# Kernel tuning notes

Measured on AMD Instinct MI355X. Metric: run time of the kernel, lower is better.

Reference implementation:

```python
import jax, jax.numpy as jnp
import numpy as np

D_MODEL = 2048
NUM_HEADS = 16
D_FF = 8192
BATCH = 4
SEQ = 2048


def setup_inputs() -> dict:
    key = jax.random.key(0)
    ks = jax.random.split(key, 16)
    s_attn = 1.0 / np.sqrt(D_MODEL)
    s_ff1 = 1.0 / np.sqrt(D_MODEL)
    s_ff2 = 1.0 / np.sqrt(D_FF)
    return {
        "x": jax.random.normal(ks[0], (BATCH, SEQ, D_MODEL), dtype=jnp.float32),
        "Wq": jax.random.normal(ks[1], (D_MODEL, D_MODEL), dtype=jnp.float32) * s_attn,
        "bq": jnp.zeros((D_MODEL,), dtype=jnp.float32),
        "Wk": jax.random.normal(ks[2], (D_MODEL, D_MODEL), dtype=jnp.float32) * s_attn,
        "bk": jnp.zeros((D_MODEL,), dtype=jnp.float32),
        "Wv": jax.random.normal(ks[3], (D_MODEL, D_MODEL), dtype=jnp.float32) * s_attn,
        "bv": jnp.zeros((D_MODEL,), dtype=jnp.float32),
        "Wo": jax.random.normal(ks[4], (D_MODEL, D_MODEL), dtype=jnp.float32) * s_attn,
        "bo": jnp.zeros((D_MODEL,), dtype=jnp.float32),
        "W1": jax.random.normal(ks[5], (D_MODEL, D_FF), dtype=jnp.float32) * s_ff1,
        "b1": jnp.zeros((D_FF,), dtype=jnp.float32),
        "W2": jax.random.normal(ks[6], (D_FF, D_MODEL), dtype=jnp.float32) * s_ff2,
        "b2": jnp.zeros((D_MODEL,), dtype=jnp.float32),
        "ln1_g": jnp.ones((D_MODEL,), dtype=jnp.float32),
        "ln1_b": jnp.zeros((D_MODEL,), dtype=jnp.float32),
        "ln2_g": jnp.ones((D_MODEL,), dtype=jnp.float32),
        "ln2_b": jnp.zeros((D_MODEL,), dtype=jnp.float32),
    }


def _layer_norm(x, g, b, eps=1e-5):
    mu = jnp.mean(x, axis=-1, keepdims=True)
    var = jnp.mean(jnp.square(x - mu), axis=-1, keepdims=True)
    return (x - mu) * jax.lax.rsqrt(var + eps) * g + b


def _attention(h, Wq, bq, Wk, bk, Wv, bv, Wo, bo):
    B, S, D = h.shape
    H = NUM_HEADS
    dk = D // H
    q = (h @ Wq + bq).reshape(B, S, H, dk).transpose(0, 2, 1, 3)  # bhsd
    k = (h @ Wk + bk).reshape(B, S, H, dk).transpose(0, 2, 1, 3)
    v = (h @ Wv + bv).reshape(B, S, H, dk).transpose(0, 2, 1, 3)
    logits = jnp.einsum("bhqd,bhkd->bhqk", q, k) / jnp.sqrt(jnp.float32(dk))
    causal = jnp.triu(jnp.ones((S, S), dtype=bool), k=1)  # True above diagonal
    logits = jnp.where(causal, -jnp.inf, logits)
    attn = jax.nn.softmax(logits, axis=-1)
    out = jnp.einsum("bhqk,bhkd->bhqd", attn, v)
    out = out.transpose(0, 2, 1, 3).reshape(B, S, D)
    return out @ Wo + bo


def reference(x, Wq, bq, Wk, bk, Wv, bv, Wo, bo, W1, b1, W2, b2,
              ln1_g, ln1_b, ln2_g, ln2_b):
    # Pre-LN attention block + residual
    h = _layer_norm(x, ln1_g, ln1_b)
    x = x + _attention(h, Wq, bq, Wk, bk, Wv, bv, Wo, bo)
    # Pre-LN FFN block + residual (GELU activation)
    h = _layer_norm(x, ln2_g, ln2_b)
    ff = jax.nn.gelu(h @ W1 + b1, approximate=False) @ W2 + b2
    return x + ff
```

## Files before the change

kernel.cpp:

```cpp
#include <hip/hip_runtime.h>
#include <hip/hip_bf16.h>

#define D_MODEL 2048
#define NUM_HEADS 16
#define D_FF 8192
#define BATCH 4
#define SEQ 2048
#define DK 128
#define MTOT (BATCH * SEQ)

typedef __attribute__((ext_vector_type(8))) short short8;
typedef __attribute__((ext_vector_type(4))) short short4v;
typedef __attribute__((ext_vector_type(4))) float f32x4;

#define MFMA16(a, b, c) __builtin_amdgcn_mfma_f32_16x16x32_bf16(a, b, c, 0, 0, 0)

#define GLOAD16(gp, lp)                                                        \
  __builtin_amdgcn_global_load_lds(                                            \
      (const __attribute__((address_space(1))) void*)(gp),                     \
      (__attribute__((address_space(3))) void*)(lp), 16, 0, 0)

#define SBAR() asm volatile("s_barrier" ::: "memory")

static __device__ __forceinline__ unsigned short f2bf(float f) {
  return __builtin_bit_cast(unsigned short, __float2bfloat16(f));
}

__global__ __launch_bounds__(256) void transpose_cvt_kernel(
    const float* __restrict__ in, __hip_bfloat16* __restrict__ out, int K, int N) {
  __shared__ float tile[32][33];
  const int n0 = blockIdx.x * 32, k0 = blockIdx.y * 32;
  const int tx = threadIdx.x & 31, ty = threadIdx.x >> 5;
#pragma unroll
  for (int i = 0; i < 4; ++i)
    tile[ty + i * 8][tx] = in[(size_t)(k0 + ty + i * 8) * N + n0 + tx];
  __syncthreads();
#pragma unroll
  for (int i = 0; i < 4; ++i)
    out[(size_t)(n0 + ty + i * 8) * K + k0 + tx] = __float2bfloat16(tile[tx][ty + i * 8]);
}

__global__ __launch_bounds__(256) void transpose_cvt4_kernel(
    const float* __restrict__ s0, const float* __restrict__ s1,
    const float* __restrict__ s2, const float* __restrict__ s3,
    __hip_bfloat16* __restrict__ d0, __hip_bfloat16* __restrict__ d1,
    __hip_bfloat16* __restrict__ d2, __hip_bfloat16* __restrict__ d3) {
  const int z = blockIdx.z;
  const float* in = z == 0 ? s0 : (z == 1 ? s1 : (z == 2 ? s2 : s3));
  __hip_bfloat16* out = z == 0 ? d0 : (z == 1 ? d1 : (z == 2 ? d2 : d3));
  __shared__ float tile[32][33];
  const int n0 = blockIdx.x * 32, k0 = blockIdx.y * 32;
  const int tx = threadIdx.x & 31, ty = threadIdx.x >> 5;
#pragma unroll
  for (int i = 0; i < 4; ++i)
    tile[ty + i * 8][tx] = in[(size_t)(k0 + ty + i * 8) * 2048 + n0 + tx];
  __syncthreads();
#pragma unroll
  for (int i = 0; i < 4; ++i)
    out[(size_t)(n0 + ty + i * 8) * 2048 + k0 + tx] =
        __float2bfloat16(tile[tx][ty + i * 8]);
}

__global__ __launch_bounds__(256) void layernorm_kernel(
    const float* __restrict__ x, const float* __restrict__ g,
    const float* __restrict__ bta, __hip_bfloat16* __restrict__ out) {
  const int row = blockIdx.x;
  const int tid = threadIdx.x;
  const float* xr = x + (size_t)row * D_MODEL;
  float4 v0 = *(const float4*)(xr + tid * 8);
  float4 v1 = *(const float4*)(xr + tid * 8 + 4);
  float s = v0.x + v0.y + v0.z + v0.w + v1.x + v1.y + v1.z + v1.w;
  float q = v0.x * v0.x + v0.y * v0.y + v0.z * v0.z + v0.w * v0.w +
            v1.x * v1.x + v1.y * v1.y + v1.z * v1.z + v1.w * v1.w;
#pragma unroll
  for (int off = 1; off < 64; off <<= 1) {
    s += __shfl_xor(s, off);
    q += __shfl_xor(q, off);
  }
  __shared__ float rs[4], rq[4];
  if ((tid & 63) == 0) {
    rs[tid >> 6] = s;
    rq[tid >> 6] = q;
  }
  __syncthreads();
  s = rs[0] + rs[1] + rs[2] + rs[3];
  q = rq[0] + rq[1] + rq[2] + rq[3];
  const float mu = s * (1.0f / D_MODEL);
  const float var = q * (1.0f / D_MODEL) - mu * mu;
  const float rstd = rsqrtf(var + 1e-5f);
  float4 g0 = *(const float4*)(g + tid * 8);
  float4 g1 = *(const float4*)(g + tid * 8 + 4);
  float4 b0 = *(const float4*)(bta + tid * 8);
  float4 b1 = *(const float4*)(bta + tid * 8 + 4);
  short8 o;
  o[0] = (short)f2bf((v0.x - mu) * rstd * g0.x + b0.x);
  o[1] = (short)f2bf((v0.y - mu) * rstd * g0.y + b0.y);
  o[2] = (short)f2bf((v0.z - mu) * rstd * g0.z + b0.z);
  o[3] = (short)f2bf((v0.w - mu) * rstd * g0.w + b0.w);
  o[4] = (short)f2bf((v1.x - mu) * rstd * g1.x + b1.x);
  o[5] = (short)f2bf((v1.y - mu) * rstd * g1.y + b1.y);
  o[6] = (short)f2bf((v1.z - mu) * rstd * g1.z + b1.z);
  o[7] = (short)f2bf((v1.w - mu) * rstd * g1.w + b1.w);
  *(short8*)(out + (size_t)row * D_MODEL + tid * 8) = o;
}

enum { EPI_BF16 = 0, EPI_VT = 1, EPI_RESID = 2, EPI_GELU = 3, EPI_QKV = 4 };

#define AF_MFMA_PHASE(FI0)                                                     \
  {                                                                            \
    const int raA = wm + (FI0) * 16 + l15;                                     \
    const int raB = wm + ((FI0) + 1) * 16 + l15;                               \
    short8 aA0 = *(const short8*)(db + raA * 128 + ((lg ^ (raA & 7)) << 4));   \
    short8 aB0 = *(const short8*)(db + raB * 128 + ((lg ^ (raB & 7)) << 4));   \
    short8 aA1 =                                                               \
        *(const short8*)(db + raA * 128 + (((4 + lg) ^ (raA & 7)) << 4));      \
    short8 aB1 =                                                               \
        *(const short8*)(db + raB * 128 + (((4 + lg) ^ (raB & 7)) << 4));      \
    SBAR();                                                                    \
    asm volatile("s_waitcnt lgkmcnt(0)" ::: "memory");                         \
    __builtin_amdgcn_sched_barrier(0);                                         \
    __builtin_amdgcn_s_setprio(1);                                             \
    _Pragma("unroll") for (int fj = 0; fj < 4; ++fj)                           \
        acc[FI0][fj] = MFMA16(aA0, bf0[fj], acc[FI0][fj]);                     \
    _Pragma("unroll") for (int fj = 0; fj < 4; ++fj)                           \
        acc[(FI0) + 1][fj] = MFMA16(aB0, bf0[fj], acc[(FI0) + 1][fj]);         \
    _Pragma("unroll") for (int fj = 0; fj < 4; ++fj)                           \
        acc[FI0][fj] = MFMA16(aA1, bf1[fj], acc[FI0][fj]);                     \
    _Pragma("unroll") for (int fj = 0; fj < 4; ++fj)                           \
        acc[(FI0) + 1][fj] = MFMA16(aB1, bf1[fj], acc[(FI0) + 1][fj]);         \
    __builtin_amdgcn_s_setprio(0);                                             \
  }

template <int EPI>
__global__ __launch_bounds__(512, 2) void gemm_kernel(
    const __hip_bfloat16* __restrict__ A, const __hip_bfloat16* __restrict__ Bt,
    const float* __restrict__ bias, const float* __restrict__ bias2,
    const float* __restrict__ bias3, const float* __restrict__ resid,
    void* __restrict__ outv, void* __restrict__ out2, void* __restrict__ out3,
    int M, int N, int K) {
  __shared__ __align__(16) unsigned char lds[2][65536];
  const int tid = threadIdx.x;
  const int lane = tid & 63, w = tid >> 6;
  const int l15 = lane & 15, lg = lane >> 4;
  const int d = blockIdx.x;
  const int x = d & 7;
  const int i = d >> 3;
  const int cC = (i & 7) + 8 * (i >> 5);
  const int rC = x + 8 * ((i >> 3) & 3);
  const int m0 = rC * 256, n0 = cC * 256;
  const int wm = (w >> 2) * 128, wn = (w & 3) * 64;

  f32x4 acc[8][4] = {};

  const int row8 = lane >> 3;
  const int g8 = (lane & 7) ^ row8;
  const int wa = (w & 3) + ((w >> 2) * 16);

  auto stA = [&](int tt, int c) {
    GLOAD16(A + (size_t)(m0 + c * 8 + row8) * K + (size_t)tt * 64 + g8 * 8,
            lds[tt & 1] + c * 1024);
  };
  auto stB = [&](int tt, int c) {
    GLOAD16(Bt + (size_t)(n0 + c * 8 + row8) * K + (size_t)tt * 64 + g8 * 8,
            lds[tt & 1] + 32768 + c * 1024);
  };

  const int nt = K >> 6;

  stB(0, w); stB(0, 8 + w); stA(0, wa);
  stB(0, 16 + w); stB(0, 24 + w); stA(0, wa + 4);
  stA(0, wa + 8); stA(0, wa + 12);
  stB(1, w); stB(1, 8 + w); stA(1, wa);
  stB(1, 16 + w); stB(1, 24 + w); stA(1, wa + 4);
  stA(1, wa + 8);
  asm volatile("s_waitcnt vmcnt(7)" ::: "memory");
  SBAR();

  for (int t = 0; t < nt; ++t) {
    const unsigned char* db = lds[t & 1];
    const bool s1 = (t + 1 < nt), s2 = (t + 2 < nt);
    short8 bf0[4], bf1[4];
    if (s1) stA(t + 1, wa + 12);
#pragma unroll
    for (int f = 0; f < 4; ++f) {
      const int rb = wn + f * 16 + l15;
      bf0[f] = *(const short8*)(db + 32768 + rb * 128 + ((lg ^ (rb & 7)) << 4));
      bf1[f] =
          *(const short8*)(db + 32768 + rb * 128 + (((4 + lg) ^ (rb & 7)) << 4));
    }
    AF_MFMA_PHASE(0)
    SBAR();
    if (s2) { stB(t + 2, w); stB(t + 2, 8 + w); stA(t + 2, wa); }
    AF_MFMA_PHASE(2)
    SBAR();
    if (s2) { stB(t + 2, 16 + w); stB(t + 2, 24 + w); stA(t + 2, wa + 4); }
    AF_MFMA_PHASE(4)
    SBAR();
    if (s2) stA(t + 2, wa + 8);
    AF_MFMA_PHASE(6)
    if (s2)
      asm volatile("s_waitcnt vmcnt(7)" ::: "memory");
    else
      asm volatile("s_waitcnt vmcnt(0)" ::: "memory");
    SBAR();
  }

#pragma unroll
  for (int fi = 0; fi < 8; ++fi) {
#pragma unroll
    for (int fj = 0; fj < 4; ++fj) {
      const int mb = m0 + wm + fi * 16 + lg * 4;
      const int n = n0 + wn + fj * 16 + l15;
      if constexpr (EPI == EPI_QKV) {
        const int sec = n >> 11;
        const int nn = n & 2047;
        const float bv = sec == 0 ? bias[nn] : (sec == 1 ? bias2[nn] : bias3[nn]);
        if (sec < 2) {
          __hip_bfloat16* o = sec == 0 ? (__hip_bfloat16*)outv : (__hip_bfloat16*)out2;
#pragma unroll
          for (int r = 0; r < 4; ++r)
            o[(size_t)(mb + r) * 2048 + nn] = __float2bfloat16(acc[fi][fj][r] + bv);
        } else {
          const int bb = mb >> 11, ss = mb & (SEQ - 1);
          const int hh = nn >> 7, dd = nn & (DK - 1);
          short4v pk;
#pragma unroll
          for (int r = 0; r < 4; ++r) pk[r] = (short)f2bf(acc[fi][fj][r] + bv);
          __hip_bfloat16* o = (__hip_bfloat16*)out3;
          *(short4v*)(o + ((size_t)((bb * NUM_HEADS + hh) * DK + dd)) * SEQ + ss) = pk;
        }
      } else {
        const float bv = bias ? bias[n] : 0.0f;
        if constexpr (EPI == EPI_VT) {
          const int bb = mb >> 11, ss = mb & (SEQ - 1);
          const int hh = n >> 7, dd = n & (DK - 1);
          short4v pk;
#pragma unroll
          for (int r = 0; r < 4; ++r) pk[r] = (short)f2bf(acc[fi][fj][r] + bv);
          __hip_bfloat16* o = (__hip_bfloat16*)outv;
          *(short4v*)(o + ((size_t)((bb * NUM_HEADS + hh) * DK + dd)) * SEQ + ss) = pk;
        } else {
#pragma unroll
          for (int r = 0; r < 4; ++r) {
            const int m = mb + r;
            const float v = acc[fi][fj][r] + bv;
            if constexpr (EPI == EPI_BF16) {
              ((__hip_bfloat16*)outv)[(size_t)m * N + n] = __float2bfloat16(v);
            } else if constexpr (EPI == EPI_GELU) {
              const float ge = 0.5f * v * (1.0f + erff(v * 0.70710678118654752f));
              ((__hip_bfloat16*)outv)[(size_t)m * N + n] = __float2bfloat16(ge);
            } else {
              ((float*)outv)[(size_t)m * N + n] = resid[(size_t)m * N + n] + v;
            }
          }
        }
      }
    }
  }
}

__global__ __launch_bounds__(512, 4) void attn_kernel(
    const __hip_bfloat16* __restrict__ Qm, const __hip_bfloat16* __restrict__ Km,
    const __hip_bfloat16* __restrict__ Vt, __hip_bfloat16* __restrict__ Om) {
  __shared__ __align__(16) unsigned char Kl[2][16384];
  __shared__ __align__(16) unsigned char Vl[2][16384];
  const int tid = threadIdx.x;
  const int lane = tid & 63, w = tid >> 6;
  const int l15 = lane & 15, lg = lane >> 4;
  const int bh = blockIdx.y, b = bh >> 4, h = bh & 15;
  const int q0 = ((int)gridDim.x - 1 - (int)blockIdx.x) * 128;
  const int qw = q0 + w * 16;
  const int row8 = lane >> 3;
  const int nt = (q0 >> 6) + 2;

  short8 qf[4];
  const __hip_bfloat16* qbase = Qm + (size_t)(b * SEQ + qw + l15) * D_MODEL + h * DK;
#pragma unroll
  for (int ks = 0; ks < 4; ++ks) qf[ks] = *(const short8*)(qbase + ks * 32 + lg * 8);

  float m_run = -1e30f, l_run = 0.0f;
  f32x4 acc_o[8];
#pragma unroll
  for (int fd = 0; fd < 8; ++fd) acc_o[fd] = (f32x4){0.f, 0.f, 0.f, 0.f};

  auto STAGE = [&](int tt) {
    unsigned char* kb = Kl[tt & 1];
    unsigned char* vb = Vl[tt & 1];
    const int t0s = tt * 64;
#pragma unroll
    for (int i = 0; i < 2; ++i) {
      const int c = w * 2 + i;
      const int row = c * 4 + lg;
      const int gcb = l15 ^ (row & 7);
      GLOAD16(Km + (size_t)(b * SEQ + t0s + row) * D_MODEL + h * DK + gcb * 8,
              kb + c * 1024);
    }
#pragma unroll
    for (int i = 0; i < 2; ++i) {
      const int c = w * 2 + i;
      const int row = c * 8 + row8;
      const int gcb = (lane & 7) ^ (row & 7);
      GLOAD16(Vt + (size_t)(bh * DK + row) * SEQ + t0s + gcb * 8, vb + c * 1024);
    }
  };

  STAGE(0);
  for (int t = 0; t < nt; ++t) {
    const int t0 = t * 64;
    if (t + 1 < nt) {
      STAGE(t + 1);
      asm volatile("s_waitcnt vmcnt(4)" ::: "memory");
    } else {
      asm volatile("s_waitcnt vmcnt(0)" ::: "memory");
    }
    SBAR();
    if (t0 <= qw + 15) {
      const unsigned char* kb = Kl[t & 1];
      const unsigned char* vb = Vl[t & 1];
      f32x4 sacc[4];
#pragma unroll
      for (int fn = 0; fn < 4; ++fn) sacc[fn] = (f32x4){0.f, 0.f, 0.f, 0.f};
      __builtin_amdgcn_s_setprio(1);
#pragma unroll
      for (int ks = 0; ks < 4; ++ks) {
        const int cb = ks * 4 + lg;
#pragma unroll
        for (int fn = 0; fn < 4; ++fn) {
          const int rn = fn * 16 + l15;
          short8 kf = *(const short8*)(kb + rn * 256 + ((cb ^ (rn & 7)) << 4));
          sacc[fn] = MFMA16(kf, qf[ks], sacc[fn]);
        }
      }
      __builtin_amdgcn_s_setprio(0);
      const float scale = 0.088388347648318447f;
      const int qg = qw + l15;
      float mt = -1e30f;
#pragma unroll
      for (int fn = 0; fn < 4; ++fn) {
        const int keyb = t0 + fn * 16 + lg * 4;
#pragma unroll
        for (int r = 0; r < 4; ++r) {
          float sv = sacc[fn][r] * scale;
          sv = (keyb + r <= qg) ? sv : -1e30f;
          sacc[fn][r] = sv;
          mt = fmaxf(mt, sv);
        }
      }
      mt = fmaxf(mt, __shfl_xor(mt, 16));
      mt = fmaxf(mt, __shfl_xor(mt, 32));
      const bool defer = __all(mt <= m_run + 8.0f);
      float alpha = 1.0f;
      if (!defer) {
        const float mnew = fmaxf(m_run, mt);
        alpha = __expf(m_run - mnew);
        m_run = mnew;
      }
      float ls = 0.0f;
#pragma unroll
      for (int fn = 0; fn < 4; ++fn)
#pragma unroll
        for (int r = 0; r < 4; ++r) {
          const float p = __expf(sacc[fn][r] - m_run);
          sacc[fn][r] = p;
          ls += p;
        }
      ls += __shfl_xor(ls, 16);
      ls += __shfl_xor(ls, 32);
      l_run = (defer ? l_run : l_run * alpha) + ls;
      if (!defer) {
        float abr[4];
#pragma unroll
        for (int r = 0; r < 4; ++r) abr[r] = __shfl(alpha, lg * 4 + r);
#pragma unroll
        for (int fd = 0; fd < 8; ++fd)
#pragma unroll
          for (int r = 0; r < 4; ++r) acc_o[fd][r] *= abr[r];
      }
      const int srcLo = l15 + 16 * (2 * (lg & 1));
      const int srcHi = srcLo + 16;
      const int hi = lg >> 1;
#pragma unroll
      for (int s = 0; s < 2; ++s) {
        short8 pf;
#pragma unroll
        for (int j = 0; j < 4; ++j) {
          const float v0 = __shfl(sacc[2 * s][j], srcLo);
          const float v1 = __shfl(sacc[2 * s + 1][j], srcLo);
          pf[j] = (short)f2bf(hi ? v1 : v0);
          const float w0 = __shfl(sacc[2 * s][j], srcHi);
          const float w1 = __shfl(sacc[2 * s + 1][j], srcHi);
          pf[4 + j] = (short)f2bf(hi ? w1 : w0);
        }
        const int cb = s * 4 + lg;
        __builtin_amdgcn_s_setprio(1);
#pragma unroll
        for (int fd = 0; fd < 8; ++fd) {
          const int rv = fd * 16 + l15;
          short8 vf = *(const short8*)(vb + rv * 128 + ((cb ^ (rv & 7)) << 4));
          acc_o[fd] = MFMA16(pf, vf, acc_o[fd]);
        }
        __builtin_amdgcn_s_setprio(0);
      }
    }
    asm volatile("s_waitcnt lgkmcnt(0)" ::: "memory");
    SBAR();
  }
  float linv[4];
#pragma unroll
  for (int r = 0; r < 4; ++r) linv[r] = __shfl(l_run, lg * 4 + r);
#pragma unroll
  for (int r = 0; r < 4; ++r) {
    const float inv = 1.0f / linv[r];
    const int qg = qw + lg * 4 + r;
    __hip_bfloat16* ob = Om + (size_t)(b * SEQ + qg) * D_MODEL + h * DK + l15;
#pragma unroll
    for (int fd = 0; fd < 8; ++fd)
      ob[fd * 16] = __float2bfloat16(acc_o[fd][r] * inv);
  }
}

extern "C" void kernel_launch(void* const* d_in, const int* in_sizes, int n_in,
                              void* d_out, int out_size, void* d_ws, size_t ws_size,
                              hipStream_t stream) {
  (void)in_sizes; (void)n_in; (void)out_size;
  const size_t MB = 1024 * 1024;
  if (ws_size < 192 * MB) return;

  const float* x  = (const float*)d_in[0];
  const float* Wq = (const float*)d_in[1];
  const float* bq = (const float*)d_in[2];
  const float* Wk = (const float*)d_in[3];
  const float* bk = (const float*)d_in[4];
  const float* Wv = (const float*)d_in[5];
  const float* bv = (const float*)d_in[6];
  const float* Wo = (const float*)d_in[7];
  const float* bo = (const float*)d_in[8];
  const float* W1 = (const float*)d_in[9];
  const float* b1 = (const float*)d_in[10];
  const float* W2 = (const float*)d_in[11];
  const float* b2 = (const float*)d_in[12];
  const float* g1 = (const float*)d_in[13];
  const float* be1 = (const float*)d_in[14];
  const float* g2 = (const float*)d_in[15];
  const float* be2 = (const float*)d_in[16];

  char* ws = (char*)d_ws;
  __hip_bfloat16* Hb  = (__hip_bfloat16*)(ws + 0 * MB);
  __hip_bfloat16* Qb  = (__hip_bfloat16*)(ws + 32 * MB);
  __hip_bfloat16* Kb  = (__hip_bfloat16*)(ws + 64 * MB);
  __hip_bfloat16* Vtb = (__hip_bfloat16*)(ws + 96 * MB);
  __hip_bfloat16* AOb = (__hip_bfloat16*)(ws + 128 * MB);
  __hip_bfloat16* FF1 = (__hip_bfloat16*)(ws + 32 * MB);
  __hip_bfloat16* WqkvT = (__hip_bfloat16*)(ws + 160 * MB);
  __hip_bfloat16* WqT = (__hip_bfloat16*)(ws + 160 * MB);
  __hip_bfloat16* WkT = (__hip_bfloat16*)(ws + 168 * MB);
  __hip_bfloat16* WvT = (__hip_bfloat16*)(ws + 176 * MB);
  __hip_bfloat16* WoT = (__hip_bfloat16*)(ws + 184 * MB);
  __hip_bfloat16* W1T = (__hip_bfloat16*)(ws + 160 * MB);
  __hip_bfloat16* W2T = (__hip_bfloat16*)(ws + 160 * MB);
  float* X2 = (float*)d_out;

  const dim3 tb(256);
  transpose_cvt4_kernel<<<dim3(64, 64, 4), tb, 0, stream>>>(
      Wq, Wk, Wv, Wo, WqT, WkT, WvT, WoT);

  layernorm_kernel<<<MTOT, tb, 0, stream>>>(x, g1, be1, Hb);

  gemm_kernel<EPI_QKV><<<768, 512, 0, stream>>>(
      Hb, WqkvT, bq, bk, bv, nullptr, Qb, Kb, Vtb, MTOT, 6144, 2048);

  attn_kernel<<<dim3(SEQ / 128, BATCH * NUM_HEADS), dim3(512), 0, stream>>>(Qb, Kb, Vtb, AOb);

  gemm_kernel<EPI_RESID><<<256, 512, 0, stream>>>(
      AOb, WoT, bo, nullptr, nullptr, x, X2, nullptr, nullptr, MTOT, 2048, 2048);

  layernorm_kernel<<<MTOT, tb, 0, stream>>>(X2, g2, be2, Hb);

  transpose_cvt_kernel<<<dim3(256, 64), tb, 0, stream>>>(W1, W1T, 2048, 8192);
  gemm_kernel<EPI_GELU><<<1024, 512, 0, stream>>>(
      Hb, W1T, b1, nullptr, nullptr, nullptr, FF1, nullptr, nullptr, MTOT, 8192, 2048);
  transpose_cvt_kernel<<<dim3(64, 256), tb, 0, stream>>>(W2, W2T, 8192, 2048);
  gemm_kernel<EPI_RESID><<<256, 512, 0, stream>>>(
      FF1, W2T, b2, nullptr, nullptr, X2, X2, nullptr, nullptr, MTOT, 2048, 8192);
}
```

Before: 1.178 ms.

## Shrink GEMM tiles to 256x128 with K=32 steps and higher occupancy

```diff
diff --git a/kernel.cpp b/kernel.cpp
--- a/kernel.cpp
+++ b/kernel.cpp
@@ -104,41 +104,16 @@
   *(short8*)(out + (size_t)row * D_MODEL + tid * 8) = o;
 }
 
-enum { EPI_BF16 = 0, EPI_VT = 1, EPI_RESID = 2, EPI_GELU = 3, EPI_QKV = 4 };
-
-#define AF_MFMA_PHASE(FI0)                                                     \
-  {                                                                            \
-    const int raA = wm + (FI0) * 16 + l15;                                     \
-    const int raB = wm + ((FI0) + 1) * 16 + l15;                               \
-    short8 aA0 = *(const short8*)(db + raA * 128 + ((lg ^ (raA & 7)) << 4));   \
-    short8 aB0 = *(const short8*)(db + raB * 128 + ((lg ^ (raB & 7)) << 4));   \
-    short8 aA1 =                                                               \
-        *(const short8*)(db + raA * 128 + (((4 + lg) ^ (raA & 7)) << 4));      \
-    short8 aB1 =                                                               \
-        *(const short8*)(db + raB * 128 + (((4 + lg) ^ (raB & 7)) << 4));      \
-    SBAR();                                                                    \
-    asm volatile("s_waitcnt lgkmcnt(0)" ::: "memory");                         \
-    __builtin_amdgcn_sched_barrier(0);                                         \
-    __builtin_amdgcn_s_setprio(1);                                             \
-    _Pragma("unroll") for (int fj = 0; fj < 4; ++fj)                           \
-        acc[FI0][fj] = MFMA16(aA0, bf0[fj], acc[FI0][fj]);                     \
-    _Pragma("unroll") for (int fj = 0; fj < 4; ++fj)                           \
-        acc[(FI0) + 1][fj] = MFMA16(aB0, bf0[fj], acc[(FI0) + 1][fj]);         \
-    _Pragma("unroll") for (int fj = 0; fj < 4; ++fj)                           \
-        acc[FI0][fj] = MFMA16(aA1, bf1[fj], acc[FI0][fj]);                     \
-    _Pragma("unroll") for (int fj = 0; fj < 4; ++fj)                           \
-        acc[(FI0) + 1][fj] = MFMA16(aB1, bf1[fj], acc[(FI0) + 1][fj]);         \
-    __builtin_amdgcn_s_setprio(0);                                             \
-  }
+enum { EPI_BF16 = 0, EPI_RESID = 2, EPI_GELU = 3, EPI_QKV = 4 };
 
 template <int EPI>
-__global__ __launch_bounds__(512, 2) void gemm_kernel(
+__global__ __launch_bounds__(512, 4) void gemm_kernel(
     const __hip_bfloat16* __restrict__ A, const __hip_bfloat16* __restrict__ Bt,
     const float* __restrict__ bias, const float* __restrict__ bias2,
     const float* __restrict__ bias3, const float* __restrict__ resid,
     void* __restrict__ outv, void* __restrict__ out2, void* __restrict__ out3,
     int M, int N, int K) {
-  __shared__ __align__(16) unsigned char lds[2][65536];
+  __shared__ __align__(16) unsigned char lds[2][24576];
   const int tid = threadIdx.x;
   const int lane = tid & 63, w = tid >> 6;
   const int l15 = lane & 15, lg = lane >> 4;
@@ -147,66 +122,55 @@
   const int i = d >> 3;
   const int cC = (i & 7) + 8 * (i >> 5);
   const int rC = x + 8 * ((i >> 3) & 3);
-  const int m0 = rC * 256, n0 = cC * 256;
-  const int wm = (w >> 2) * 128, wn = (w & 3) * 64;
-
-  f32x4 acc[8][4] = {};
-
-  const int row8 = lane >> 3;
-  const int g8 = (lane & 7) ^ row8;
-  const int wa = (w & 3) + ((w >> 2) * 16);
+  const int m0 = rC * 256, n0 = cC * 128;
+  const int wm = (w >> 1) * 64, wn = (w & 1) * 64;
+
+  f32x4 acc[4][4] = {};
+
+  const int rsub = lane >> 2;
+  const int gblk = (lane & 3) ^ (rsub & 3);
 
   auto stA = [&](int tt, int c) {
-    GLOAD16(A + (size_t)(m0 + c * 8 + row8) * K + (size_t)tt * 64 + g8 * 8,
+    GLOAD16(A + (size_t)(m0 + c * 16 + rsub) * K + (size_t)tt * 32 + gblk * 8,
             lds[tt & 1] + c * 1024);
   };
   auto stB = [&](int tt, int c) {
-    GLOAD16(Bt + (size_t)(n0 + c * 8 + row8) * K + (size_t)tt * 64 + g8 * 8,
-            lds[tt & 1] + 32768 + c * 1024);
+    GLOAD16(Bt + (size_t)(n0 + c * 16 + rsub) * K + (size_t)tt * 32 + gblk * 8,
+            lds[tt & 1] + 16384 + c * 1024);
   };
-
-  const int nt = K >> 6;
-
-  stB(0, w); stB(0, 8 + w); stA(0, wa);
-  stB(0, 16 + w); stB(0, 24 + w); stA(0, wa + 4);
-  stA(0, wa + 8); stA(0, wa + 12);
-  stB(1, w); stB(1, 8 + w); stA(1, wa);
-  stB(1, 16 + w); stB(1, 24 + w); stA(1, wa + 4);
-  stA(1, wa + 8);
-  asm volatile("s_waitcnt vmcnt(7)" ::: "memory");
-  SBAR();
-
+  auto STAGE = [&](int tt) { stA(tt, 2 * w); stA(tt, 2 * w + 1); stB(tt, w); };
+
+  const int nt = K >> 5;
+  STAGE(0);
+  STAGE(1);
   for (int t = 0; t < nt; ++t) {
-    const unsigned char* db = lds[t & 1];
-    const bool s1 = (t + 1 < nt), s2 = (t + 2 < nt);
-    short8 bf0[4], bf1[4];
-    if (s1) stA(t + 1, wa + 12);
-#pragma unroll
-    for (int f = 0; f < 4; ++f) {
-      const int rb = wn + f * 16 + l15;
-      bf0[f] = *(const short8*)(db + 32768 + rb * 128 + ((lg ^ (rb & 7)) << 4));
-      bf1[f] =
-          *(const short8*)(db + 32768 + rb * 128 + (((4 + lg) ^ (rb & 7)) << 4));
-    }
-    AF_MFMA_PHASE(0)
-    SBAR();
-    if (s2) { stB(t + 2, w); stB(t + 2, 8 + w); stA(t + 2, wa); }
-    AF_MFMA_PHASE(2)
-    SBAR();
-    if (s2) { stB(t + 2, 16 + w); stB(t + 2, 24 + w); stA(t + 2, wa + 4); }
-    AF_MFMA_PHASE(4)
-    SBAR();
-    if (s2) stA(t + 2, wa + 8);
-    AF_MFMA_PHASE(6)
-    if (s2)
-      asm volatile("s_waitcnt vmcnt(7)" ::: "memory");
+    if (t + 1 < nt)
+      asm volatile("s_waitcnt vmcnt(3)" ::: "memory");
     else
       asm volatile("s_waitcnt vmcnt(0)" ::: "memory");
     SBAR();
-  }
-
-#pragma unroll
-  for (int fi = 0; fi < 8; ++fi) {
+    const unsigned char* db = lds[t & 1];
+    short8 af[4], bf[4];
+#pragma unroll
+    for (int f = 0; f < 4; ++f) {
+      const int ra = wm + f * 16 + l15;
+      af[f] = *(const short8*)(db + ra * 64 + ((lg ^ (ra & 3)) << 4));
+      const int rb = wn + f * 16 + l15;
+      bf[f] = *(const short8*)(db + 16384 + rb * 64 + ((lg ^ (rb & 3)) << 4));
+    }
+    __builtin_amdgcn_s_setprio(1);
+#pragma unroll
+    for (int fi = 0; fi < 4; ++fi)
+#pragma unroll
+      for (int fj = 0; fj < 4; ++fj)
+        acc[fi][fj] = MFMA16(af[fi], bf[fj], acc[fi][fj]);
+    __builtin_amdgcn_s_setprio(0);
+    SBAR();
+    if (t + 2 < nt) STAGE(t + 2);
+  }
+
+#pragma unroll
+  for (int fi = 0; fi < 4; ++fi) {
 #pragma unroll
     for (int fj = 0; fj < 4; ++fj) {
       const int mb = m0 + wm + fi * 16 + lg * 4;
@@ -231,27 +195,17 @@
         }
       } else {
         const float bv = bias ? bias[n] : 0.0f;
-        if constexpr (EPI == EPI_VT) {
-          const int bb = mb >> 11, ss = mb & (SEQ - 1);
-          const int hh = n >> 7, dd = n & (DK - 1);
-          short4v pk;
-#pragma unroll
-          for (int r = 0; r < 4; ++r) pk[r] = (short)f2bf(acc[fi][fj][r] + bv);
-          __hip_bfloat16* o = (__hip_bfloat16*)outv;
-          *(short4v*)(o + ((size_t)((bb * NUM_HEADS + hh) * DK + dd)) * SEQ + ss) = pk;
-        } else {
-#pragma unroll
-          for (int r = 0; r < 4; ++r) {
-            const int m = mb + r;
-            const float v = acc[fi][fj][r] + bv;
-            if constexpr (EPI == EPI_BF16) {
-              ((__hip_bfloat16*)outv)[(size_t)m * N + n] = __float2bfloat16(v);
-            } else if constexpr (EPI == EPI_GELU) {
-              const float ge = 0.5f * v * (1.0f + erff(v * 0.70710678118654752f));
-              ((__hip_bfloat16*)outv)[(size_t)m * N + n] = __float2bfloat16(ge);
-            } else {
-              ((float*)outv)[(size_t)m * N + n] = resid[(size_t)m * N + n] + v;
-            }
+#pragma unroll
+        for (int r = 0; r < 4; ++r) {
+          const int m = mb + r;
+          const float v = acc[fi][fj][r] + bv;
+          if constexpr (EPI == EPI_BF16) {
+            ((__hip_bfloat16*)outv)[(size_t)m * N + n] = __float2bfloat16(v);
+          } else if constexpr (EPI == EPI_GELU) {
+            const float ge = 0.5f * v * (1.0f + erff(v * 0.70710678118654752f));
+            ((__hip_bfloat16*)outv)[(size_t)m * N + n] = __float2bfloat16(ge);
+          } else {
+            ((float*)outv)[(size_t)m * N + n] = resid[(size_t)m * N + n] + v;
           }
         }
       }
@@ -466,20 +420,20 @@
 
   layernorm_kernel<<<MTOT, tb, 0, stream>>>(x, g1, be1, Hb);
 
-  gemm_kernel<EPI_QKV><<<768, 512, 0, stream>>>(
+  gemm_kernel<EPI_QKV><<<1536, 512, 0, stream>>>(
       Hb, WqkvT, bq, bk, bv, nullptr, Qb, Kb, Vtb, MTOT, 6144, 2048);
 
   attn_kernel<<<dim3(SEQ / 128, BATCH * NUM_HEADS), dim3(512), 0, stream>>>(Qb, Kb, Vtb, AOb);
 
-  gemm_kernel<EPI_RESID><<<256, 512, 0, stream>>>(
+  gemm_kernel<EPI_RESID><<<512, 512, 0, stream>>>(
       AOb, WoT, bo, nullptr, nullptr, x, X2, nullptr, nullptr, MTOT, 2048, 2048);
 
   layernorm_kernel<<<MTOT, tb, 0, stream>>>(X2, g2, be2, Hb);
 
   transpose_cvt_kernel<<<dim3(256, 64), tb, 0, stream>>>(W1, W1T, 2048, 8192);
-  gemm_kernel<EPI_GELU><<<1024, 512, 0, stream>>>(
+  gemm_kernel<EPI_GELU><<<2048, 512, 0, stream>>>(
       Hb, W1T, b1, nullptr, nullptr, nullptr, FF1, nullptr, nullptr, MTOT, 8192, 2048);
   transpose_cvt_kernel<<<dim3(64, 256), tb, 0, stream>>>(W2, W2T, 8192, 2048);
-  gemm_kernel<EPI_RESID><<<256, 512, 0, stream>>>(
+  gemm_kernel<EPI_RESID><<<512, 512, 0, stream>>>(
       FF1, W2T, b2, nullptr, nullptr, X2, X2, nullptr, nullptr, MTOT, 2048, 8192);
 }
```

Result: slower. 1.243 ms (+5.5%).
